# Optimization experiments

Measured on AMD Instinct MI355X. Metric: run time of the kernel, lower is better.

The kernel has to match this reference:

```python
import jax, jax.numpy as jnp
import numpy as np

D_MODEL, D_STATE, D_CONV, EXPAND = 1024, 16, 4, 2
D_INNER = D_MODEL * EXPAND
B, T = 1, 2048
EPS = 1e-5


def setup_inputs() -> dict:
    key = jax.random.key(0)
    ks = jax.random.split(key, 8)
    x = jax.random.normal(ks[0], (B, T, D_MODEL), dtype=jnp.float32)
    W_in = jax.random.normal(ks[1], (D_MODEL, 2 * D_INNER), dtype=jnp.float32) * 0.02
    conv_w = jax.random.normal(ks[2], (D_INNER, D_CONV), dtype=jnp.float32) * 0.2
    conv_b = jax.random.normal(ks[3], (D_INNER,), dtype=jnp.float32) * 0.02
    W_x = jax.random.normal(ks[4], (D_INNER, 2 * D_STATE + 1), dtype=jnp.float32) * 0.02
    W_dt = jax.random.normal(ks[5], (1, D_INNER), dtype=jnp.float32) * 0.5
    b_dt = jax.random.uniform(ks[6], (D_INNER,), dtype=jnp.float32, minval=-0.001, maxval=0.001)
    A_log = jnp.broadcast_to(jnp.log(jnp.arange(1, D_STATE + 1, dtype=jnp.float32))[None, :], (D_INNER, D_STATE))
    Dparam = jnp.ones((D_INNER,), dtype=jnp.float32)
    W_out = jax.random.normal(ks[7], (D_INNER, D_MODEL), dtype=jnp.float32) * 0.02
    ln_g = jnp.ones((D_MODEL,), dtype=jnp.float32)
    ln_b = jnp.zeros((D_MODEL,), dtype=jnp.float32)
    return {"x": x, "W_in": W_in, "conv_w": conv_w, "conv_b": conv_b, "W_x": W_x,
            "W_dt": W_dt, "b_dt": b_dt, "A_log": A_log, "D": Dparam,
            "W_out": W_out, "ln_g": ln_g, "ln_b": ln_b}


def _silu(v):
    return v * jax.nn.sigmoid(v)


def _layernorm(v, g, b):
    mu = jnp.mean(v, axis=-1, keepdims=True)
    var = jnp.mean((v - mu) ** 2, axis=-1, keepdims=True)
    return (v - mu) * jax.lax.rsqrt(var + EPS) * g + b


def _causal_depthwise_conv(xp, conv_w, conv_b):
    # xp: (B, T, D_INNER) -> (B, D_INNER, T) with left pad of D_CONV-1
    xc = jnp.swapaxes(xp, 1, 2)
    xc = jnp.pad(xc, ((0, 0), (0, 0), (D_CONV - 1, 0)))
    w = conv_w[:, None, :]  # (O=D_INNER, I/groups=1, K)
    out = jax.lax.conv_general_dilated(
        xc, w, window_strides=(1,), padding='VALID',
        dimension_numbers=('NCH', 'OIH', 'NCH'), feature_group_count=D_INNER)
    return jnp.swapaxes(out + conv_b[None, :, None], 1, 2)  # (B, T, D_INNER)


def reference(x, W_in, conv_w, conv_b, W_x, W_dt, b_dt, A_log, D, W_out, ln_g, ln_b):
    residual = x
    xn = _layernorm(x, ln_g, ln_b)
    xz = xn @ W_in                      # (B, T, 2*D_INNER)
    x_proj, z = jnp.split(xz, 2, axis=-1)
    x_conv = _silu(_causal_depthwise_conv(x_proj, conv_w, conv_b))  # (B, T, D_INNER)

    ssm = x_conv @ W_x                  # (B, T, 1 + 2*D_STATE)
    dt_raw = ssm[..., :1]
    Bp = ssm[..., 1:1 + D_STATE]        # (B, T, D_STATE)
    Cp = ssm[..., 1 + D_STATE:]         # (B, T, D_STATE)
    dt = jax.nn.softplus(dt_raw @ W_dt + b_dt)  # (B, T, D_INNER)

    A = -jnp.exp(A_log)                 # (D_INNER, D_STATE)
    A_bar = jnp.exp(dt[..., None] * A)                              # (B,T,d,n)
    Bx = dt[..., None] * Bp[:, :, None, :] * x_conv[..., None]      # (B,T,d,n)

    def step(h, inp):
        Ab_t, Bx_t, C_t = inp           # (B,d,n),(B,d,n),(B,n)
        h = Ab_t * h + Bx_t
        y_t = jnp.einsum('bdn,bn->bd', h, C_t)
        return h, y_t

    h0 = jnp.zeros((x.shape[0], D_INNER, D_STATE), dtype=x.dtype)
    _, ys = jax.lax.scan(step, h0, (jnp.swapaxes(A_bar, 0, 1),
                                    jnp.swapaxes(Bx, 0, 1),
                                    jnp.swapaxes(Cp, 0, 1)))
    y = jnp.swapaxes(ys, 0, 1)          # (B, T, D_INNER)

    y = y + x_conv * D
    y = y * _silu(z)
    return y @ W_out + residual
```

## Files before the change

### kernel.cpp

```cpp
#include <hip/hip_runtime.h>
#include <hip/hip_bf16.h>

typedef __hip_bfloat16 bf16;
typedef __attribute__((ext_vector_type(8))) short bf16x8;
typedef __attribute__((ext_vector_type(4))) float f32x4;

#define T_LEN 2048
#define DMODEL 1024
#define DINNER 2048
#define DSTATE 16
#define LN_EPS 1e-5f
#define NCHUNK 128
#define CLEN 16
#define SSTR 64
#define PSEG 131072

#define GLOBAL_AS __attribute__((address_space(1)))
#define LDS_AS __attribute__((address_space(3)))

__device__ __forceinline__ void g2l16(void* lds, const void* g) {
    __builtin_amdgcn_global_load_lds((const GLOBAL_AS void*)g, (LDS_AS void*)lds, 16, 0, 0);
}

__device__ __forceinline__ float b2f(short s) {
    return __uint_as_float(((unsigned)(unsigned short)s) << 16);
}

__global__ void prep_all(const float* __restrict__ Win, const float* __restrict__ Wout,
                         const float* __restrict__ Wx, const float* __restrict__ x,
                         const float* __restrict__ lng, const float* __restrict__ lnb,
                         bf16* __restrict__ WinT, bf16* __restrict__ WoutT,
                         bf16* __restrict__ WxT, bf16* __restrict__ xn) {
    __shared__ float t[32][33];
    int bid = blockIdx.x, tid = threadIdx.x;
    int tx = tid & 31, ty4 = (tid >> 5) * 4;
    if (bid < 4096) {
        int n0 = (bid & 127) * 32, k0 = (bid >> 7) * 32;
#pragma unroll
        for (int r = 0; r < 4; r++)
            t[ty4 + r][tx] = Win[(size_t)(k0 + ty4 + r) * 4096 + n0 + tx];
        __syncthreads();
#pragma unroll
        for (int r = 0; r < 4; r++)
            WinT[(size_t)(n0 + ty4 + r) * 1024 + k0 + tx] = __float2bfloat16(t[tx][ty4 + r]);
    } else if (bid < 6144) {
        int b = bid - 4096;
        int n0 = (b & 31) * 32, k0 = (b >> 5) * 32;
#pragma unroll
        for (int r = 0; r < 4; r++)
            t[ty4 + r][tx] = Wout[(size_t)(k0 + ty4 + r) * 1024 + n0 + tx];
        __syncthreads();
#pragma unroll
        for (int r = 0; r < 4; r++)
            WoutT[(size_t)(n0 + ty4 + r) * 2048 + k0 + tx] = __float2bfloat16(t[tx][ty4 + r]);
    } else if (bid < 6656) {
        int idx = (bid - 6144) * 256 + tid;
        int n = idx >> 11, k = idx & 2047;
        WxT[idx] = __float2bfloat16(n < 33 ? Wx[k * 33 + n] : 0.f);
    } else {
        int row = bid - 6656;
        const float* xr = x + (size_t)row * DMODEL;
        float v[4];
        float s = 0.f, q = 0.f;
#pragma unroll
        for (int i = 0; i < 4; i++) {
            v[i] = xr[tid + i * 256];
            s += v[i];
            q += v[i] * v[i];
        }
        __shared__ float sh_s[256], sh_q[256];
        sh_s[tid] = s; sh_q[tid] = q;
        __syncthreads();
        for (int st = 128; st > 0; st >>= 1) {
            if (tid < st) { sh_s[tid] += sh_s[tid + st]; sh_q[tid] += sh_q[tid + st]; }
            __syncthreads();
        }
        float mean = sh_s[0] * (1.f / DMODEL);
        float var  = sh_q[0] * (1.f / DMODEL) - mean * mean;
        float rstd = rsqrtf(var + LN_EPS);
#pragma unroll
        for (int i = 0; i < 4; i++) {
            int c = tid + i * 256;
            xn[(size_t)row * DMODEL + c] =
                __float2bfloat16((v[i] - mean) * rstd * lng[c] + lnb[c]);
        }
    }
}

template <int BM, int BN, int WAVE_M, int WAVE_N, int WRITE_RESID, int OUT_BF16>
__global__ void gemm_mfma(const bf16* __restrict__ A, const bf16* __restrict__ Bt,
                          void* __restrict__ Cv, const float* __restrict__ resid,
                          int M, int N, int Kslice, int lda) {
    constexpr int WMsz = BM / WAVE_M;
    constexpr int WNsz = BN / WAVE_N;
    constexpr int TM = WMsz / 16;
    constexpr int TN = WNsz / 16;
    __shared__ short As[BM * 64];
    __shared__ short Bs[BN * 64];
    int tid = threadIdx.x;
    int lane = tid & 63, wave = tid >> 6;
    int wm = (wave / WAVE_N) * WMsz, wn = (wave % WAVE_N) * WNsz;
    int rowBase = blockIdx.y * BM, colBase = blockIdx.x * BN;
    int kbase = blockIdx.z * Kslice;

    f32x4 acc[TM][TN];
#pragma unroll
    for (int i = 0; i < TM; i++)
#pragma unroll
        for (int j = 0; j < TN; j++) acc[i][j] = f32x4{0.f, 0.f, 0.f, 0.f};

    int srow = tid >> 3;
    int cc = (tid & 7) ^ (srow & 7);
    const int ldsoff = tid * 16;

    for (int k0 = kbase; k0 < kbase + Kslice; k0 += 64) {
#pragma unroll
        for (int j = 0; j < BM / 32; j++)
            g2l16((char*)As + j * 4096 + ldsoff,
                  A + (size_t)(rowBase + j * 32 + srow) * lda + k0 + cc * 8);
#pragma unroll
        for (int j = 0; j < BN / 32; j++)
            g2l16((char*)Bs + j * 4096 + ldsoff,
                  Bt + (size_t)(colBase + j * 32 + srow) * lda + k0 + cc * 8);
        __syncthreads();
#pragma unroll
        for (int ks = 0; ks < 2; ks++) {
            bf16x8 af[TM], bfr[TN];
#pragma unroll
            for (int i = 0; i < TM; i++) {
                int row = wm + i * 16 + (lane & 15);
                int slot = (ks * 4 + (lane >> 4)) ^ (row & 7);
                af[i] = *(const bf16x8*)((const char*)As + row * 128 + slot * 16);
            }
#pragma unroll
            for (int j = 0; j < TN; j++) {
                int row = wn + j * 16 + (lane & 15);
                int slot = (ks * 4 + (lane >> 4)) ^ (row & 7);
                bfr[j] = *(const bf16x8*)((const char*)Bs + row * 128 + slot * 16);
            }
#pragma unroll
            for (int i = 0; i < TM; i++)
#pragma unroll
                for (int j = 0; j < TN; j++)
                    acc[i][j] = __builtin_amdgcn_mfma_f32_16x16x32_bf16(
                        af[i], bfr[j], acc[i][j], 0, 0, 0);
        }
        __syncthreads();
    }
    int rq = lane >> 4, cn = lane & 15;
    float* Cf = (float*)Cv + (size_t)blockIdx.z * M * N;
#pragma unroll
    for (int i = 0; i < TM; i++) {
#pragma unroll
        for (int j = 0; j < TN; j++) {
#pragma unroll
            for (int r = 0; r < 4; r++) {
                size_t row = rowBase + wm + i * 16 + rq * 4 + r;
                int col = colBase + wn + j * 16 + cn;
                float v = acc[i][j][r];
                if (WRITE_RESID) v += resid[row * N + col];
                if (OUT_BF16)
                    ((bf16*)Cv)[row * N + col] = __float2bfloat16(v);
                else
                    Cf[row * N + col] = v;
            }
        }
    }
}

__global__ void conv_silu(const bf16* __restrict__ xz, const float* __restrict__ cw,
                          const float* __restrict__ cb, bf16* __restrict__ xc) {
    int idx = blockIdx.x * 256 + threadIdx.x;
    int t = idx >> 11, d = idx & (DINNER - 1);
    float acc = cb[d];
#pragma unroll
    for (int k = 0; k < 4; k++) {
        int tt = t - 3 + k;
        if (tt >= 0) acc += (float)xz[(size_t)tt * (2 * DINNER) + d] * cw[d * 4 + k];
    }
    xc[idx] = __float2bfloat16(acc / (1.f + __expf(-acc)));
}

__device__ __forceinline__ float softplus_f(float pre) {
    return (pre > 20.f) ? pre : log1pf(__expf(pre));
}

__device__ __forceinline__ void powtree(float q, float* a) {
    a[0] = q;
    a[1] = q * q;
    a[2] = a[1] * q;
    a[3] = a[1] * a[1];
#pragma unroll
    for (int j = 0; j < 4; j++) a[4 + j] = a[j] * a[3];
#pragma unroll
    for (int j = 0; j < 8; j++) a[8 + j] = a[j] * a[7];
}

__device__ __forceinline__ void fill_slab(float (*slab)[SSTR], const float* parts,
                                          int t0, int tid) {
#pragma unroll
    for (int r = 0; r < 4; r++) {
        int idx = r * 256 + tid;
        int off = (t0 << 6) + idx;
        slab[idx >> 6][idx & 63] = parts[off] + parts[off + PSEG] +
                                   parts[off + 2 * PSEG] + parts[off + 3 * PSEG];
    }
}

__global__ __launch_bounds__(256, 4) void scan_pass1(
        const float* __restrict__ parts, const bf16* __restrict__ xc,
        const float* __restrict__ Wdt, const float* __restrict__ bdt,
        const float* __restrict__ Alog,
        float* __restrict__ P, float* __restrict__ S) {
    __shared__ float slab[CLEN][SSTR];
    __shared__ short xcs[CLEN][256];
    int tid = threadIdx.x;
    int d = blockIdx.x * 256 + tid;
    int c = blockIdx.y;
    int t0 = c * CLEN;
    fill_slab(slab, parts, t0, tid);
#pragma unroll
    for (int i = 0; i < CLEN; i++)
        xcs[i][tid] = ((const short*)xc)[(size_t)(t0 + i) * DINNER + d];
    float A[DSTATE], Pv[DSTATE], Sv[DSTATE];
    bool fast = true;
#pragma unroll
    for (int n = 0; n < DSTATE; n++) {
        A[n] = -__expf(Alog[d * DSTATE + n]);
        fast = fast && (fabsf(A[n] + (float)(n + 1)) < 1e-3f * (n + 1));
        Pv[n] = 1.f; Sv[n] = 0.f;
    }
    float wdt = Wdt[d], bd = bdt[d];
    __syncthreads();
    if (fast) {
        for (int i = 0; i < CLEN; i++) {
            float dt = softplus_f(slab[i][0] * wdt + bd);
            float dtxc = dt * b2f(xcs[i][tid]);
            float a[DSTATE];
            powtree(__expf(-dt), a);
#pragma unroll
            for (int n = 0; n < DSTATE; n++) {
                Pv[n] *= a[n];
                Sv[n] = a[n] * Sv[n] + dtxc * slab[i][1 + n];
            }
        }
    } else {
        for (int i = 0; i < CLEN; i++) {
            float dt = softplus_f(slab[i][0] * wdt + bd);
            float dtxc = dt * b2f(xcs[i][tid]);
#pragma unroll
            for (int n = 0; n < DSTATE; n++) {
                float a = __expf(dt * A[n]);
                Pv[n] *= a;
                Sv[n] = a * Sv[n] + dtxc * slab[i][1 + n];
            }
        }
    }
    size_t base = (size_t)c * DINNER * DSTATE + d;
#pragma unroll
    for (int n = 0; n < DSTATE; n++) {
        P[base + (size_t)n * DINNER] = Pv[n];
        S[base + (size_t)n * DINNER] = Sv[n];
    }
}

__global__ void scan_pass2(float* __restrict__ P, const float* __restrict__ S) {
    int idx = blockIdx.x * 256 + threadIdx.x;
    float H = 0.f;
#pragma unroll 4
    for (int c = 0; c < NCHUNK; c++) {
        size_t o = (size_t)c * DINNER * DSTATE + idx;
        float Pc = P[o], Sc = S[o];
        P[o] = H;
        H = Pc * H + Sc;
    }
}

__global__ __launch_bounds__(256, 4) void scan_pass3(
        const float* __restrict__ parts, const bf16* __restrict__ xc,
        const bf16* __restrict__ xz,
        const float* __restrict__ Wdt, const float* __restrict__ bdt,
        const float* __restrict__ Alog, const float* __restrict__ Dp,
        const float* __restrict__ Hst, bf16* __restrict__ yf) {
    __shared__ float slab[CLEN][SSTR];
    __shared__ short xcs[CLEN][256];
    __shared__ short zs[CLEN][256];
    int tid = threadIdx.x;
    int d = blockIdx.x * 256 + tid;
    int c = blockIdx.y;
    int t0 = c * CLEN;
    fill_slab(slab, parts, t0, tid);
#pragma unroll
    for (int i = 0; i < CLEN; i++) {
        xcs[i][tid] = ((const short*)xc)[(size_t)(t0 + i) * DINNER + d];
        zs[i][tid]  = ((const short*)xz)[(size_t)(t0 + i) * (2 * DINNER) + DINNER + d];
    }
    float A[DSTATE], h[DSTATE];
    bool fast = true;
    size_t base = (size_t)c * DINNER * DSTATE + d;
#pragma unroll
    for (int n = 0; n < DSTATE; n++) {
        A[n] = -__expf(Alog[d * DSTATE + n]);
        fast = fast && (fabsf(A[n] + (float)(n + 1)) < 1e-3f * (n + 1));
        h[n] = Hst[base + (size_t)n * DINNER];
    }
    float wdt = Wdt[d], bd = bdt[d], Dd = Dp[d];
    __syncthreads();
    if (fast) {
        for (int i = 0; i < CLEN; i++) {
            float dt = softplus_f(slab[i][0] * wdt + bd);
            float xcv = b2f(xcs[i][tid]);
            float dtxc = dt * xcv;
            float a[DSTATE];
            powtree(__expf(-dt), a);
            float y0 = 0.f, y1 = 0.f, y2 = 0.f, y3 = 0.f;
#pragma unroll
            for (int n = 0; n < 4; n++) {
                h[n] = a[n] * h[n] + dtxc * slab[i][1 + n];
                y0 += h[n] * slab[i][17 + n];
                h[n + 4] = a[n + 4] * h[n + 4] + dtxc * slab[i][5 + n];
                y1 += h[n + 4] * slab[i][21 + n];
                h[n + 8] = a[n + 8] * h[n + 8] + dtxc * slab[i][9 + n];
                y2 += h[n + 8] * slab[i][25 + n];
                h[n + 12] = a[n + 12] * h[n + 12] + dtxc * slab[i][13 + n];
                y3 += h[n + 12] * slab[i][29 + n];
            }
            float y = (y0 + y1) + (y2 + y3);
            float z = b2f(zs[i][tid]);
            float sz = z / (1.f + __expf(-z));
            yf[(size_t)(t0 + i) * DINNER + d] = __float2bfloat16((y + xcv * Dd) * sz);
        }
    } else {
        for (int i = 0; i < CLEN; i++) {
            float dt = softplus_f(slab[i][0] * wdt + bd);
            float xcv = b2f(xcs[i][tid]);
            float dtxc = dt * xcv;
            float y = 0.f;
#pragma unroll
            for (int n = 0; n < DSTATE; n++) {
                float a = __expf(dt * A[n]);
                h[n] = a * h[n] + dtxc * slab[i][1 + n];
                y += h[n] * slab[i][17 + n];
            }
            float z = b2f(zs[i][tid]);
            float sz = z / (1.f + __expf(-z));
            yf[(size_t)(t0 + i) * DINNER + d] = __float2bfloat16((y + xcv * Dd) * sz);
        }
    }
}

extern "C" void kernel_launch(void* const* d_in, const int* in_sizes, int n_in,
                              void* d_out, int out_size, void* d_ws, size_t ws_size,
                              hipStream_t stream) {
    const float* x     = (const float*)d_in[0];
    const float* W_in  = (const float*)d_in[1];
    const float* convw = (const float*)d_in[2];
    const float* convb = (const float*)d_in[3];
    const float* W_x   = (const float*)d_in[4];
    const float* W_dt  = (const float*)d_in[5];
    const float* b_dt  = (const float*)d_in[6];
    const float* A_log = (const float*)d_in[7];
    const float* Dp    = (const float*)d_in[8];
    const float* W_out = (const float*)d_in[9];
    const float* ln_g  = (const float*)d_in[10];
    const float* ln_b  = (const float*)d_in[11];
    float* out = (float*)d_out;

    char* wsb = (char*)d_ws;
    bf16*  xn    = (bf16*)(wsb);
    bf16*  WinT  = (bf16*)(wsb + (4ull  << 20));
    bf16*  WoutT = (bf16*)(wsb + (12ull << 20));
    bf16*  WxT   = (bf16*)(wsb + (16ull << 20));
    bf16*  xz    = (bf16*)(wsb + (17ull << 20));
    bf16*  xc    = (bf16*)(wsb + (33ull << 20));
    float* parts = (float*)(wsb + (41ull << 20));
    float* P     = (float*)(wsb + (44ull << 20));
    float* S     = (float*)(wsb + (60ull << 20));
    bf16*  yf    = (bf16*)(wsb + (76ull << 20));

    prep_all<<<8704, 256, 0, stream>>>(W_in, W_out, W_x, x, ln_g, ln_b,
                                       WinT, WoutT, WxT, xn);

    gemm_mfma<128, 128, 2, 2, 0, 1><<<dim3(4096 / 128, 2048 / 128), 256, 0, stream>>>(
        xn, WinT, xz, nullptr, 2048, 4096, 1024, 1024);

    conv_silu<<<(T_LEN * DINNER) / 256, 256, 0, stream>>>(xz, convw, convb, xc);

    gemm_mfma<32, 64, 2, 2, 0, 0><<<dim3(1, 2048 / 32, 4), 256, 0, stream>>>(
        xc, WxT, parts, nullptr, 2048, 64, 512, 2048);

    scan_pass1<<<dim3(DINNER / 256, NCHUNK), 256, 0, stream>>>(
        parts, xc, W_dt, b_dt, A_log, P, S);
    scan_pass2<<<(DINNER * DSTATE) / 256, 256, 0, stream>>>(P, S);
    scan_pass3<<<dim3(DINNER / 256, NCHUNK), 256, 0, stream>>>(
        parts, xc, xz, W_dt, b_dt, A_log, Dp, P, yf);

    gemm_mfma<64, 64, 2, 2, 1, 0><<<dim3(1024 / 64, 2048 / 64), 256, 0, stream>>>(
        yf, WoutT, out, x, 2048, 1024, 2048, 2048);
}
```

Measured before the change: 248.7 us.

## Reformulate chunked scan via cumulative dt, vectorize conv, drop LDS staging

Pass 1 of the chunked selective scan now stores only the per-channel dt sum for each chunk, plus the state contribution weighted by exp(A*(Ltot-Lc)). It no longer keeps a per-state decay product, and pass 2 rebuilds the chunk decay from A and that sum. This halves pass-1 output writes and removes the sequential product chain. The depthwise conv now handles four channels per thread with vector loads and stores. The scan kernels keep xc, z and precomputed dt in registers instead of LDS, and the W_x columns are realigned so B and C slices start at offsets 4 and 20. Risks are higher register pressure from the fully unrolled loops and extra exp work in pass 2.

```diff
diff --git a/kernel.cpp b/kernel.cpp
--- a/kernel.cpp
+++ b/kernel.cpp
@@ -24,6 +24,11 @@
 
 __device__ __forceinline__ float b2f(short s) {
     return __uint_as_float(((unsigned)(unsigned short)s) << 16);
+}
+
+__device__ __forceinline__ unsigned short f2bu(float f) {
+    bf16 b = __float2bfloat16(f);
+    return *reinterpret_cast<unsigned short*>(&b);
 }
 
 __global__ void prep_all(const float* __restrict__ Win, const float* __restrict__ Wout,
@@ -56,7 +61,8 @@
     } else if (bid < 6656) {
         int idx = (bid - 6144) * 256 + tid;
         int n = idx >> 11, k = idx & 2047;
-        WxT[idx] = __float2bfloat16(n < 33 ? Wx[k * 33 + n] : 0.f);
+        int j = (n == 0) ? 0 : (n >= 4 && n <= 35) ? n - 3 : -1;
+        WxT[idx] = __float2bfloat16(j >= 0 ? Wx[k * 33 + j] : 0.f);
     } else {
         int row = bid - 6656;
         const float* xr = x + (size_t)row * DMODEL;
@@ -171,14 +177,28 @@
 __global__ void conv_silu(const bf16* __restrict__ xz, const float* __restrict__ cw,
                           const float* __restrict__ cb, bf16* __restrict__ xc) {
     int idx = blockIdx.x * 256 + threadIdx.x;
-    int t = idx >> 11, d = idx & (DINNER - 1);
-    float acc = cb[d];
+    int t = idx >> 9, d4 = (idx & 511) * 4;
+    const f32x4 bv = *(const f32x4*)(cb + d4);
+    float acc0 = bv[0], acc1 = bv[1], acc2 = bv[2], acc3 = bv[3];
+    const f32x4* cwv = (const f32x4*)(cw + d4 * 4);
+    f32x4 w0 = cwv[0], w1 = cwv[1], w2 = cwv[2], w3 = cwv[3];
 #pragma unroll
     for (int k = 0; k < 4; k++) {
         int tt = t - 3 + k;
-        if (tt >= 0) acc += (float)xz[(size_t)tt * (2 * DINNER) + d] * cw[d * 4 + k];
-    }
-    xc[idx] = __float2bfloat16(acc / (1.f + __expf(-acc)));
+        if (tt >= 0) {
+            ushort4 v = *(const ushort4*)((const short*)xz + (size_t)tt * (2 * DINNER) + d4);
+            acc0 = fmaf(b2f((short)v.x), w0[k], acc0);
+            acc1 = fmaf(b2f((short)v.y), w1[k], acc1);
+            acc2 = fmaf(b2f((short)v.z), w2[k], acc2);
+            acc3 = fmaf(b2f((short)v.w), w3[k], acc3);
+        }
+    }
+    ushort4 o;
+    o.x = f2bu(acc0 / (1.f + __expf(-acc0)));
+    o.y = f2bu(acc1 / (1.f + __expf(-acc1)));
+    o.z = f2bu(acc2 / (1.f + __expf(-acc2)));
+    o.w = f2bu(acc3 / (1.f + __expf(-acc3)));
+    *(ushort4*)((short*)xc + (size_t)t * DINNER + d4) = o;
 }
 
 __device__ __forceinline__ float softplus_f(float pre) {
@@ -211,68 +231,78 @@
         const float* __restrict__ parts, const bf16* __restrict__ xc,
         const float* __restrict__ Wdt, const float* __restrict__ bdt,
         const float* __restrict__ Alog,
-        float* __restrict__ P, float* __restrict__ S) {
+        float* __restrict__ Ld, float* __restrict__ S) {
     __shared__ float slab[CLEN][SSTR];
-    __shared__ short xcs[CLEN][256];
     int tid = threadIdx.x;
     int d = blockIdx.x * 256 + tid;
     int c = blockIdx.y;
     int t0 = c * CLEN;
     fill_slab(slab, parts, t0, tid);
+    short xcv[CLEN];
 #pragma unroll
     for (int i = 0; i < CLEN; i++)
-        xcs[i][tid] = ((const short*)xc)[(size_t)(t0 + i) * DINNER + d];
-    float A[DSTATE], Pv[DSTATE], Sv[DSTATE];
+        xcv[i] = ((const short*)xc)[(size_t)(t0 + i) * DINNER + d];
+    float A[DSTATE];
     bool fast = true;
 #pragma unroll
     for (int n = 0; n < DSTATE; n++) {
         A[n] = -__expf(Alog[d * DSTATE + n]);
         fast = fast && (fabsf(A[n] + (float)(n + 1)) < 1e-3f * (n + 1));
-        Pv[n] = 1.f; Sv[n] = 0.f;
     }
     float wdt = Wdt[d], bd = bdt[d];
     __syncthreads();
+    float dtv[CLEN];
+#pragma unroll
+    for (int i = 0; i < CLEN; i++)
+        dtv[i] = softplus_f(slab[i][0] * wdt + bd);
+    float Lc[CLEN];
+    float run = 0.f;
+#pragma unroll
+    for (int i = 0; i < CLEN; i++) { run += dtv[i]; Lc[i] = run; }
+    float Ltot = run;
+    float Sv[DSTATE];
+#pragma unroll
+    for (int n = 0; n < DSTATE; n++) Sv[n] = 0.f;
     if (fast) {
+#pragma unroll
         for (int i = 0; i < CLEN; i++) {
-            float dt = softplus_f(slab[i][0] * wdt + bd);
-            float dtxc = dt * b2f(xcs[i][tid]);
+            float u = dtv[i] * b2f(xcv[i]);
             float a[DSTATE];
-            powtree(__expf(-dt), a);
-#pragma unroll
-            for (int n = 0; n < DSTATE; n++) {
-                Pv[n] *= a[n];
-                Sv[n] = a[n] * Sv[n] + dtxc * slab[i][1 + n];
-            }
+            powtree(__expf(Lc[i] - Ltot), a);
+#pragma unroll
+            for (int n = 0; n < DSTATE; n++)
+                Sv[n] = fmaf(a[n], u * slab[i][4 + n], Sv[n]);
         }
     } else {
+#pragma unroll
         for (int i = 0; i < CLEN; i++) {
-            float dt = softplus_f(slab[i][0] * wdt + bd);
-            float dtxc = dt * b2f(xcs[i][tid]);
-#pragma unroll
-            for (int n = 0; n < DSTATE; n++) {
-                float a = __expf(dt * A[n]);
-                Pv[n] *= a;
-                Sv[n] = a * Sv[n] + dtxc * slab[i][1 + n];
-            }
-        }
-    }
+            float u = dtv[i] * b2f(xcv[i]);
+            float g = Ltot - Lc[i];
+#pragma unroll
+            for (int n = 0; n < DSTATE; n++)
+                Sv[n] = fmaf(__expf(A[n] * g), u * slab[i][4 + n], Sv[n]);
+        }
+    }
+    Ld[(size_t)c * DINNER + d] = Ltot;
     size_t base = (size_t)c * DINNER * DSTATE + d;
 #pragma unroll
-    for (int n = 0; n < DSTATE; n++) {
-        P[base + (size_t)n * DINNER] = Pv[n];
+    for (int n = 0; n < DSTATE; n++)
         S[base + (size_t)n * DINNER] = Sv[n];
-    }
-}
-
-__global__ void scan_pass2(float* __restrict__ P, const float* __restrict__ S) {
+}
+
+__global__ void scan_pass2(const float* __restrict__ Ld, const float* __restrict__ S,
+                           const float* __restrict__ Alog, float* __restrict__ Hst) {
     int idx = blockIdx.x * 256 + threadIdx.x;
+    int d = idx & (DINNER - 1), n = idx >> 11;
+    float A = -__expf(Alog[d * DSTATE + n]);
     float H = 0.f;
-#pragma unroll 4
+#pragma unroll 8
     for (int c = 0; c < NCHUNK; c++) {
         size_t o = (size_t)c * DINNER * DSTATE + idx;
-        float Pc = P[o], Sc = S[o];
-        P[o] = H;
-        H = Pc * H + Sc;
+        float Sc = S[o];
+        float a = __expf(A * Ld[(size_t)c * DINNER + d]);
+        Hst[o] = H;
+        H = a * H + Sc;
     }
 }
 
@@ -283,17 +313,16 @@
         const float* __restrict__ Alog, const float* __restrict__ Dp,
         const float* __restrict__ Hst, bf16* __restrict__ yf) {
     __shared__ float slab[CLEN][SSTR];
-    __shared__ short xcs[CLEN][256];
-    __shared__ short zs[CLEN][256];
     int tid = threadIdx.x;
     int d = blockIdx.x * 256 + tid;
     int c = blockIdx.y;
     int t0 = c * CLEN;
     fill_slab(slab, parts, t0, tid);
+    short xcv[CLEN], zv[CLEN];
 #pragma unroll
     for (int i = 0; i < CLEN; i++) {
-        xcs[i][tid] = ((const short*)xc)[(size_t)(t0 + i) * DINNER + d];
-        zs[i][tid]  = ((const short*)xz)[(size_t)(t0 + i) * (2 * DINNER) + DINNER + d];
+        xcv[i] = ((const short*)xc)[(size_t)(t0 + i) * DINNER + d];
+        zv[i]  = ((const short*)xz)[(size_t)(t0 + i) * (2 * DINNER) + DINNER + d];
     }
     float A[DSTATE], h[DSTATE];
     bool fast = true;
@@ -306,45 +335,52 @@
     }
     float wdt = Wdt[d], bd = bdt[d], Dd = Dp[d];
     __syncthreads();
+    float dtv[CLEN];
+#pragma unroll
+    for (int i = 0; i < CLEN; i++)
+        dtv[i] = softplus_f(slab[i][0] * wdt + bd);
     if (fast) {
+        float qv[CLEN];
+#pragma unroll
+        for (int i = 0; i < CLEN; i++) qv[i] = __expf(-dtv[i]);
+#pragma unroll
         for (int i = 0; i < CLEN; i++) {
-            float dt = softplus_f(slab[i][0] * wdt + bd);
-            float xcv = b2f(xcs[i][tid]);
-            float dtxc = dt * xcv;
+            float xcf = b2f(xcv[i]);
+            float u = dtv[i] * xcf;
             float a[DSTATE];
-            powtree(__expf(-dt), a);
+            powtree(qv[i], a);
             float y0 = 0.f, y1 = 0.f, y2 = 0.f, y3 = 0.f;
 #pragma unroll
             for (int n = 0; n < 4; n++) {
-                h[n] = a[n] * h[n] + dtxc * slab[i][1 + n];
-                y0 += h[n] * slab[i][17 + n];
-                h[n + 4] = a[n + 4] * h[n + 4] + dtxc * slab[i][5 + n];
-                y1 += h[n + 4] * slab[i][21 + n];
-                h[n + 8] = a[n + 8] * h[n + 8] + dtxc * slab[i][9 + n];
-                y2 += h[n + 8] * slab[i][25 + n];
-                h[n + 12] = a[n + 12] * h[n + 12] + dtxc * slab[i][13 + n];
-                y3 += h[n + 12] * slab[i][29 + n];
+                h[n]      = fmaf(a[n],      h[n],      u * slab[i][4 + n]);
+                y0 = fmaf(h[n],      slab[i][20 + n], y0);
+                h[n + 4]  = fmaf(a[n + 4],  h[n + 4],  u * slab[i][8 + n]);
+                y1 = fmaf(h[n + 4],  slab[i][24 + n], y1);
+                h[n + 8]  = fmaf(a[n + 8],  h[n + 8],  u * slab[i][12 + n]);
+                y2 = fmaf(h[n + 8],  slab[i][28 + n], y2);
+                h[n + 12] = fmaf(a[n + 12], h[n + 12], u * slab[i][16 + n]);
+                y3 = fmaf(h[n + 12], slab[i][32 + n], y3);
             }
             float y = (y0 + y1) + (y2 + y3);
-            float z = b2f(zs[i][tid]);
+            float z = b2f(zv[i]);
             float sz = z / (1.f + __expf(-z));
-            yf[(size_t)(t0 + i) * DINNER + d] = __float2bfloat16((y + xcv * Dd) * sz);
+            yf[(size_t)(t0 + i) * DINNER + d] = __float2bfloat16(fmaf(xcf, Dd, y) * sz);
         }
     } else {
+#pragma unroll
         for (int i = 0; i < CLEN; i++) {
-            float dt = softplus_f(slab[i][0] * wdt + bd);
-            float xcv = b2f(xcs[i][tid]);
-            float dtxc = dt * xcv;
+            float xcf = b2f(xcv[i]);
+            float u = dtv[i] * xcf;
             float y = 0.f;
 #pragma unroll
             for (int n = 0; n < DSTATE; n++) {
-                float a = __expf(dt * A[n]);
-                h[n] = a * h[n] + dtxc * slab[i][1 + n];
-                y += h[n] * slab[i][17 + n];
+                float a = __expf(dtv[i] * A[n]);
+                h[n] = fmaf(a, h[n], u * slab[i][4 + n]);
+                y = fmaf(h[n], slab[i][20 + n], y);
             }
-            float z = b2f(zs[i][tid]);
+            float z = b2f(zv[i]);
             float sz = z / (1.f + __expf(-z));
-            yf[(size_t)(t0 + i) * DINNER + d] = __float2bfloat16((y + xcv * Dd) * sz);
+            yf[(size_t)(t0 + i) * DINNER + d] = __float2bfloat16(fmaf(xcf, Dd, y) * sz);
         }
     }
 }
@@ -374,7 +410,8 @@
     bf16*  xz    = (bf16*)(wsb + (17ull << 20));
     bf16*  xc    = (bf16*)(wsb + (33ull << 20));
     float* parts = (float*)(wsb + (41ull << 20));
-    float* P     = (float*)(wsb + (44ull << 20));
+    float* Ld    = (float*)(wsb + (43ull << 20));
+    float* Hst   = (float*)(wsb + (44ull << 20));
     float* S     = (float*)(wsb + (60ull << 20));
     bf16*  yf    = (bf16*)(wsb + (76ull << 20));
 
@@ -384,16 +421,16 @@
     gemm_mfma<128, 128, 2, 2, 0, 1><<<dim3(4096 / 128, 2048 / 128), 256, 0, stream>>>(
         xn, WinT, xz, nullptr, 2048, 4096, 1024, 1024);
 
-    conv_silu<<<(T_LEN * DINNER) / 256, 256, 0, stream>>>(xz, convw, convb, xc);
+    conv_silu<<<(T_LEN * DINNER / 4) / 256, 256, 0, stream>>>(xz, convw, convb, xc);
 
     gemm_mfma<32, 64, 2, 2, 0, 0><<<dim3(1, 2048 / 32, 4), 256, 0, stream>>>(
         xc, WxT, parts, nullptr, 2048, 64, 512, 2048);
 
     scan_pass1<<<dim3(DINNER / 256, NCHUNK), 256, 0, stream>>>(
-        parts, xc, W_dt, b_dt, A_log, P, S);
-    scan_pass2<<<(DINNER * DSTATE) / 256, 256, 0, stream>>>(P, S);
+        parts, xc, W_dt, b_dt, A_log, Ld, S);
+    scan_pass2<<<(DINNER * DSTATE) / 256, 256, 0, stream>>>(Ld, S, A_log, Hst);
     scan_pass3<<<dim3(DINNER / 256, NCHUNK), 256, 0, stream>>>(
-        parts, xc, xz, W_dt, b_dt, A_log, Dp, P, yf);
+        parts, xc, xz, W_dt, b_dt, A_log, Dp, Hst, yf);
 
     gemm_mfma<64, 64, 2, 2, 1, 0><<<dim3(1024 / 64, 2048 / 64), 256, 0, stream>>>(
         yf, WoutT, out, x, 2048, 1024, 2048, 2048);
```

New measurement: 258.9 us. 1.04x slower.
